# Kernel tuning notes

Hardware: AMD Instinct MI355X
Metric: run time of the kernel (lower is better)

## Reference

```python
import jax, jax.numpy as jnp
import numpy as np

N_NODES = 100_000
N_EDGES = 3_200_000
IN_DIM, HID_DIM, EMB_DIM = 128, 64, 32


def setup_inputs() -> dict:
    key = jax.random.key(0)
    k0, k1, k2, k3, k4, k5 = jax.random.split(key, 6)
    x = jax.random.normal(k0, (N_NODES, IN_DIM), dtype=jnp.float32)
    edge_index = jax.random.randint(k1, (2, N_EDGES), 0, N_NODES, dtype=jnp.int32)
    # GCNConv parameters (glorot-ish scale)
    W1 = jax.random.normal(k2, (IN_DIM, HID_DIM), dtype=jnp.float32) / np.sqrt(IN_DIM)
    b1 = jnp.zeros((HID_DIM,), dtype=jnp.float32)
    W2 = jax.random.normal(k3, (HID_DIM, EMB_DIM), dtype=jnp.float32) / np.sqrt(HID_DIM)
    b2 = jnp.zeros((EMB_DIM,), dtype=jnp.float32)
    return {"x": x, "W1": W1, "b1": b1, "W2": W2, "b2": b2, "edge_index": edge_index}


def reference(x, W1, b1, W2, b2, edge_index):
    """Two-layer GCN encoder (PyG GCNConv semantics, eval mode so dropout is a no-op).

    Each GCNConv: add self-loops, symmetric deg^-1/2 normalization,
    out = scatter_add(norm_e * (x @ W)[src], dst) + b.
    """
    N = x.shape[0]
    loops = jnp.arange(N, dtype=edge_index.dtype)
    src = jnp.concatenate([edge_index[0], loops])  # [E+N]
    dst = jnp.concatenate([edge_index[1], loops])  # [E+N]

    # degree of destination nodes (self-loops guarantee deg >= 1)
    deg = jax.ops.segment_sum(jnp.ones_like(dst, dtype=jnp.float32), dst,
                              num_segments=N)
    dinv = jax.lax.rsqrt(deg)                      # deg^-1/2, finite since deg>=1
    norm = dinv[src] * dinv[dst]                   # [E+N]

    def gcn_conv(h, W, b):
        h = h @ W                                  # dense transform [N, D_out]
        msg = h[src] * norm[:, None]               # gather + scale [E+N, D_out]
        return jax.ops.segment_sum(msg, dst, num_segments=N) + b

    h = jax.nn.relu(gcn_conv(x, W1, b1))
    # F.dropout with training=False is identity -> omitted
    return gcn_conv(h, W2, b2)
```

## Files before the change

kernel.cpp:

```cpp
#include <hip/hip_runtime.h>

static constexpr int NN = 100000;
static constexpr int NE = 3200000;
static constexpr int DI = 128;
static constexpr int DH = 64;
static constexpr int DO = 32;

static constexpr int NBK  = 391;
static constexpr int BCAP = 9216;
static constexpr int TILE = 8192;
static constexpr int NEB  = (NE + TILE - 1) / TILE;
static constexpr int NEBP = 392;
static constexpr int XW1_BASE = NEB + 1;
static constexpr int XW1_BLOCKS = (NN + 63) / 64;

typedef short short8 __attribute__((ext_vector_type(8)));
typedef float f32x4  __attribute__((ext_vector_type(4)));

__device__ __forceinline__ unsigned short f2bf(float f) {
    union { float f; unsigned u; } v; v.f = f;
    unsigned r = v.u + 0x7FFFu + ((v.u >> 16) & 1u);
    return (unsigned short)(r >> 16);
}
__device__ __forceinline__ float bflo(unsigned u) {
    union { unsigned u; float f; } v; v.u = u << 16; return v.f;
}
__device__ __forceinline__ float bfhi(unsigned u) {
    union { unsigned u; float f; } v; v.u = u & 0xFFFF0000u; return v.f;
}

__global__ __launch_bounds__(256) void k_count(
        const int* __restrict__ dst, int* __restrict__ cnt) {
    __shared__ int hist[NBK];
    int tid = threadIdx.x;
    for (int i = tid; i < NBK; i += 256) hist[i] = 0;
    __syncthreads();

    int base = blockIdx.x * TILE;
    int rem = NE - base;
#pragma unroll
    for (int k4 = 0; k4 < 8; ++k4) {
        int off = tid * 32 + k4 * 4;
        if (off < rem) {
            int4 d4 = *(const int4*)(dst + base + off);
            atomicAdd(&hist[(unsigned)d4.x >> 8], 1);
            atomicAdd(&hist[(unsigned)d4.y >> 8], 1);
            atomicAdd(&hist[(unsigned)d4.z >> 8], 1);
            atomicAdd(&hist[(unsigned)d4.w >> 8], 1);
        }
    }
    __syncthreads();
    for (int i = tid; i < NBK; i += 256)
        cnt[i * NEBP + blockIdx.x] = hist[i];
}

__global__ __launch_bounds__(64) void k_scan(
        int* __restrict__ cnt, int* __restrict__ bcur) {
    int b = blockIdx.x, tid = threadIdx.x;
    int* row = cnt + b * NEBP;
    int carry = 0;
    for (int c = 0; c < (NEB + 63) / 64; ++c) {
        int idx = c * 64 + tid;
        int v = (idx < NEB) ? row[idx] : 0;
        int inc = v;
#pragma unroll
        for (int o = 1; o < 64; o <<= 1) {
            int u = __shfl_up(inc, o, 64);
            if (tid >= o) inc += u;
        }
        int tot = __shfl(inc, 63, 64);
        if (idx < NEB) row[idx] = carry + inc - v;
        carry += tot;
    }
    if (tid == 0) bcur[b] = carry;
}

__global__ __launch_bounds__(256) void k_mega(
        const int* __restrict__ src, const int* __restrict__ dst,
        const int* __restrict__ gposM, int* __restrict__ bstore,
        const float* __restrict__ x, const float* __restrict__ W1,
        const float* __restrict__ W2,
        unsigned short* __restrict__ w2bf, unsigned short* __restrict__ h1b) {
    __shared__ int lcur[NBK];

    int tid = threadIdx.x;

    if (blockIdx.x < NEB) {
        for (int i = tid; i < NBK; i += 256)
            lcur[i] = gposM[i * NEBP + blockIdx.x];
        __syncthreads();

        int base = blockIdx.x * TILE;
        int rem = NE - base;
#pragma unroll
        for (int k4 = 0; k4 < 8; ++k4) {
            int off = tid * 32 + k4 * 4;
            if (off < rem) {
                int4 s4 = *(const int4*)(src + base + off);
                int4 d4 = *(const int4*)(dst + base + off);
                int b0 = (unsigned)d4.x >> 8, p0 = ((d4.x & 255) << 24) | s4.x;
                int b1 = (unsigned)d4.y >> 8, p1 = ((d4.y & 255) << 24) | s4.y;
                int b2 = (unsigned)d4.z >> 8, p2 = ((d4.z & 255) << 24) | s4.z;
                int b3 = (unsigned)d4.w >> 8, p3 = ((d4.w & 255) << 24) | s4.w;
                int o0 = atomicAdd(&lcur[b0], 1);
                int o1 = atomicAdd(&lcur[b1], 1);
                int o2 = atomicAdd(&lcur[b2], 1);
                int o3 = atomicAdd(&lcur[b3], 1);
                if (o0 < BCAP) bstore[b0 * BCAP + o0] = p0;
                if (o1 < BCAP) bstore[b1 * BCAP + o1] = p1;
                if (o2 < BCAP) bstore[b2 * BCAP + o2] = p2;
                if (o3 < BCAP) bstore[b3 * BCAP + o3] = p3;
            }
        }
    } else if (blockIdx.x == NEB) {
        for (int i = tid; i < DH * DO; i += 256) w2bf[i] = f2bf(W2[i]);
    } else {
        int wave = tid >> 6, lane = tid & 63;
        int q = lane >> 4, m = lane & 15, o0 = wave * 16;
        int nb = (blockIdx.x - XW1_BASE) * 64;

        short8 bfr[4];
#pragma unroll
        for (int kb = 0; kb < 4; ++kb)
#pragma unroll
            for (int j = 0; j < 8; ++j)
                bfr[kb][j] = (short)f2bf(W1[(kb * 32 + q * 8 + j) * DH + o0 + m]);

#pragma unroll
        for (int mt = 0; mt < 4; ++mt) {
            int row = min(nb + mt * 16 + m, NN - 1);
            const float* xr = x + (size_t)row * DI;
            f32x4 acc = {0.f, 0.f, 0.f, 0.f};
#pragma unroll
            for (int kb = 0; kb < 4; ++kb) {
                f32x4 u0 = *(const f32x4*)(xr + kb * 32 + q * 8);
                f32x4 u1 = *(const f32x4*)(xr + kb * 32 + q * 8 + 4);
                short8 a;
                a[0] = (short)f2bf(u0.x); a[1] = (short)f2bf(u0.y);
                a[2] = (short)f2bf(u0.z); a[3] = (short)f2bf(u0.w);
                a[4] = (short)f2bf(u1.x); a[5] = (short)f2bf(u1.y);
                a[6] = (short)f2bf(u1.z); a[7] = (short)f2bf(u1.w);
                acc = __builtin_amdgcn_mfma_f32_16x16x32_bf16(a, bfr[kb], acc, 0, 0, 0);
            }
#pragma unroll
            for (int r = 0; r < 4; ++r) {
                int n = nb + mt * 16 + q * 4 + r;
                if (n < NN) h1b[(size_t)n * DH + o0 + m] = f2bf(acc[r]);
            }
        }
    }
}

__global__ __launch_bounds__(512) void k_bsort(
        const int* __restrict__ bcur, int* __restrict__ bstore,
        int* __restrict__ rpb, int* __restrict__ rpe, float* __restrict__ dinv,
        unsigned* __restrict__ h1) {
    __shared__ int buf[BCAP];
    __shared__ int sorted[BCAP];
    __shared__ int hist[256], scan[256], cur[256];
    __shared__ float sdinv[256];

    int b = blockIdx.x, tid = threadIdx.x;
    int cnt = min(bcur[b], BCAP);
    int base = b * BCAP;
    for (int i = tid; i < cnt; i += 512) buf[i] = bstore[base + i];
    if (tid < 256) hist[tid] = 0;
    __syncthreads();
    for (int i = tid; i < cnt; i += 512)
        atomicAdd(&hist[((unsigned)buf[i]) >> 24], 1);
    __syncthreads();

    if (tid < 64) {
        int carry = 0;
        for (int c = 0; c < 4; ++c) {
            int idx = c * 64 + tid;
            int v = hist[idx];
            int inc = v;
#pragma unroll
            for (int o = 1; o < 64; o <<= 1) {
                int u = __shfl_up(inc, o, 64);
                if (tid >= o) inc += u;
            }
            int tot = __shfl(inc, 63, 64);
            scan[idx] = carry + inc - v;
            cur[idx]  = carry + inc - v;
            carry += tot;
        }
    }
    __syncthreads();

    if (tid < 256) {
        int n = b * 256 + tid;
        if (n < NN) {
            int beg = base + scan[tid];
            rpb[n] = beg;
            rpe[n] = beg + hist[tid];
            float dv = rsqrtf(1.0f + (float)hist[tid]);
            dinv[n] = dv;
            sdinv[tid] = dv;
        }
    }

    for (int i = tid; i < cnt; i += 512) {
        unsigned pv = (unsigned)buf[i];
        int pos = atomicAdd(&cur[pv >> 24], 1);
        sorted[pos] = (int)(pv & 0xFFFFFF);
    }
    __syncthreads();
    for (int i = tid; i < cnt; i += 512) bstore[base + i] = sorted[i];

    for (int i = tid; i < 2048; i += 512) {
        int r = i >> 3, n = b * 256 + r;
        if (n < NN) {
            float dv = sdinv[r];
            uint4* p = (uint4*)h1 + (size_t)b * 2048 + i;
            uint4 u = *p;
            u.x = (unsigned)f2bf(bflo(u.x) * dv) | ((unsigned)f2bf(bfhi(u.x) * dv) << 16);
            u.y = (unsigned)f2bf(bflo(u.y) * dv) | ((unsigned)f2bf(bfhi(u.y) * dv) << 16);
            u.z = (unsigned)f2bf(bflo(u.z) * dv) | ((unsigned)f2bf(bfhi(u.z) * dv) << 16);
            u.w = (unsigned)f2bf(bflo(u.w) * dv) | ((unsigned)f2bf(bfhi(u.w) * dv) << 16);
            *p = u;
        }
    }
}

__global__ __launch_bounds__(256) void k_gather64(
        const int* __restrict__ rpb, const int* __restrict__ rpe,
        const int* __restrict__ csr, const unsigned* __restrict__ h,
        const float* __restrict__ dinv, const float* __restrict__ b1,
        unsigned* __restrict__ tbf) {
    int wave = threadIdx.x >> 6, lane = threadIdx.x & 63;
    int q = lane >> 3, f8 = lane & 7;
    int n = blockIdx.x * 4 + wave;
    int beg = rpb[n], end = rpe[n];
    float dn = dinv[n];

    float s0 = 0.f, s1 = 0.f, s2 = 0.f, s3 = 0.f;
    float s4 = 0.f, s5 = 0.f, s6 = 0.f, s7 = 0.f;
    if (q == 0) {
        uint4 u = *(const uint4*)(h + (size_t)n * 32 + 4 * f8);
        s0 = bflo(u.x); s1 = bfhi(u.x); s2 = bflo(u.y); s3 = bfhi(u.y);
        s4 = bflo(u.z); s5 = bfhi(u.z); s6 = bflo(u.w); s7 = bfhi(u.w);
    }
#define ACC8(U)                                                         \
    s0 += bflo(U.x); s1 += bfhi(U.x); s2 += bflo(U.y); s3 += bfhi(U.y); \
    s4 += bflo(U.z); s5 += bfhi(U.z); s6 += bflo(U.w); s7 += bfhi(U.w);

    for (int c = beg; c < end; c += 64) {
        int cnt = min(64, end - c);
        int sidx = (lane < cnt) ? csr[c + lane] : 0;
        int j = 0;
        for (; j + 16 <= cnt; j += 16) {
            int sa = __shfl(sidx, j + q, 64);
            int sb = __shfl(sidx, j + 8 + q, 64);
            uint4 ua = *(const uint4*)(h + (size_t)sa * 32 + 4 * f8);
            uint4 ub = *(const uint4*)(h + (size_t)sb * 32 + 4 * f8);
            ACC8(ua) ACC8(ub)
        }
        for (; j + 8 <= cnt; j += 8) {
            int sa = __shfl(sidx, j + q, 64);
            uint4 ua = *(const uint4*)(h + (size_t)sa * 32 + 4 * f8);
            ACC8(ua)
        }
        for (; j < cnt; j += 8) {
            int slot = j + q;
            int s = __shfl(sidx, slot, 64);
            if (slot < cnt) {
                uint4 u = *(const uint4*)(h + (size_t)s * 32 + 4 * f8);
                ACC8(u)
            }
        }
    }
#undef ACC8

#define RED8(m)                                                         \
    s0 += __shfl_xor(s0, m, 64); s1 += __shfl_xor(s1, m, 64);           \
    s2 += __shfl_xor(s2, m, 64); s3 += __shfl_xor(s3, m, 64);           \
    s4 += __shfl_xor(s4, m, 64); s5 += __shfl_xor(s5, m, 64);           \
    s6 += __shfl_xor(s6, m, 64); s7 += __shfl_xor(s7, m, 64);
    RED8(8) RED8(16) RED8(32)
#undef RED8

    if (q == 0) {
        float4 bA = *(const float4*)(b1 + 8 * f8);
        float4 bB = *(const float4*)(b1 + 8 * f8 + 4);
        float t0 = fmaxf(fmaf(s0, dn, bA.x), 0.f);
        float t1 = fmaxf(fmaf(s1, dn, bA.y), 0.f);
        float t2 = fmaxf(fmaf(s2, dn, bA.z), 0.f);
        float t3 = fmaxf(fmaf(s3, dn, bA.w), 0.f);
        float t4 = fmaxf(fmaf(s4, dn, bB.x), 0.f);
        float t5 = fmaxf(fmaf(s5, dn, bB.y), 0.f);
        float t6 = fmaxf(fmaf(s6, dn, bB.z), 0.f);
        float t7 = fmaxf(fmaf(s7, dn, bB.w), 0.f);
        uint4 o;
        o.x = (unsigned)f2bf(t0) | ((unsigned)f2bf(t1) << 16);
        o.y = (unsigned)f2bf(t2) | ((unsigned)f2bf(t3) << 16);
        o.z = (unsigned)f2bf(t4) | ((unsigned)f2bf(t5) << 16);
        o.w = (unsigned)f2bf(t6) | ((unsigned)f2bf(t7) << 16);
        *(uint4*)(tbf + (size_t)n * 32 + 4 * f8) = o;
    }
}

__global__ __launch_bounds__(256) void k_l2_mfma(
        const unsigned short* __restrict__ tbf, const unsigned short* __restrict__ w2bf,
        const float* __restrict__ dinv, unsigned short* __restrict__ h2b) {
    int wave = threadIdx.x >> 6, lane = threadIdx.x & 63;
    int q = lane >> 4, m = lane & 15;
    int o0 = (wave & 1) * 16, mt = wave >> 1;
    int nb = blockIdx.x * 32;

    short8 bf[2];
#pragma unroll
    for (int kb = 0; kb < 2; ++kb)
#pragma unroll
        for (int j = 0; j < 8; ++j)
            bf[kb][j] = (short)w2bf[(kb * 32 + q * 8 + j) * DO + o0 + m];

    int row = nb + mt * 16 + m;
    f32x4 acc = {0.f, 0.f, 0.f, 0.f};
#pragma unroll
    for (int kb = 0; kb < 2; ++kb) {
        short8 a = *(const short8*)(tbf + (size_t)row * DH + kb * 32 + q * 8);
        acc = __builtin_amdgcn_mfma_f32_16x16x32_bf16(a, bf[kb], acc, 0, 0, 0);
    }
#pragma unroll
    for (int r = 0; r < 4; ++r) {
        int n = nb + mt * 16 + q * 4 + r;
        if (n < NN) h2b[(size_t)n * DO + o0 + m] = f2bf(acc[r] * dinv[n]);
    }
}

__global__ __launch_bounds__(256) void k_gather32(
        const int* __restrict__ rpb, const int* __restrict__ rpe,
        const int* __restrict__ csr, const unsigned* __restrict__ h,
        const float* __restrict__ dinv, const float* __restrict__ b2,
        float* __restrict__ out) {
    int wave = threadIdx.x >> 6, lane = threadIdx.x & 63;
    int q = lane >> 2, f4 = lane & 3;
    int n = blockIdx.x * 4 + wave;
    int beg = rpb[n], end = rpe[n];

    float s0 = 0.f, s1 = 0.f, s2 = 0.f, s3 = 0.f;
    float s4 = 0.f, s5 = 0.f, s6 = 0.f, s7 = 0.f;
    if (q == 0) {
        uint4 u = *(const uint4*)(h + (size_t)n * 16 + 4 * f4);
        s0 = bflo(u.x); s1 = bfhi(u.x); s2 = bflo(u.y); s3 = bfhi(u.y);
        s4 = bflo(u.z); s5 = bfhi(u.z); s6 = bflo(u.w); s7 = bfhi(u.w);
    }
#define ACC8(U)                                                         \
    s0 += bflo(U.x); s1 += bfhi(U.x); s2 += bflo(U.y); s3 += bfhi(U.y); \
    s4 += bflo(U.z); s5 += bfhi(U.z); s6 += bflo(U.w); s7 += bfhi(U.w);

    for (int c = beg; c < end; c += 64) {
        int cnt = min(64, end - c);
        int sidx = (lane < cnt) ? csr[c + lane] : 0;
        int j = 0;
        for (; j + 32 <= cnt; j += 32) {
            int sa = __shfl(sidx, j + q, 64);
            int sb = __shfl(sidx, j + 16 + q, 64);
            uint4 ua = *(const uint4*)(h + (size_t)sa * 16 + 4 * f4);
            uint4 ub = *(const uint4*)(h + (size_t)sb * 16 + 4 * f4);
            ACC8(ua) ACC8(ub)
        }
        for (; j + 16 <= cnt; j += 16) {
            int sa = __shfl(sidx, j + q, 64);
            uint4 ua = *(const uint4*)(h + (size_t)sa * 16 + 4 * f4);
            ACC8(ua)
        }
        for (; j < cnt; j += 16) {
            int slot = j + q;
            int s = __shfl(sidx, slot, 64);
            if (slot < cnt) {
                uint4 u = *(const uint4*)(h + (size_t)s * 16 + 4 * f4);
                ACC8(u)
            }
        }
    }
#undef ACC8

#define RED8(m)                                                         \
    s0 += __shfl_xor(s0, m, 64); s1 += __shfl_xor(s1, m, 64);           \
    s2 += __shfl_xor(s2, m, 64); s3 += __shfl_xor(s3, m, 64);           \
    s4 += __shfl_xor(s4, m, 64); s5 += __shfl_xor(s5, m, 64);           \
    s6 += __shfl_xor(s6, m, 64); s7 += __shfl_xor(s7, m, 64);
    RED8(4) RED8(8) RED8(16) RED8(32)
#undef RED8

    if (q == 0) {
        float dn = dinv[n];
        float4 bA = *(const float4*)(b2 + 8 * f4);
        float4 bB = *(const float4*)(b2 + 8 * f4 + 4);
        size_t o = (size_t)n * 32 + 8 * f4;
        float4 oA, oB;
        oA.x = fmaf(s0, dn, bA.x); oA.y = fmaf(s1, dn, bA.y);
        oA.z = fmaf(s2, dn, bA.z); oA.w = fmaf(s3, dn, bA.w);
        oB.x = fmaf(s4, dn, bB.x); oB.y = fmaf(s5, dn, bB.y);
        oB.z = fmaf(s6, dn, bB.z); oB.w = fmaf(s7, dn, bB.w);
        *(float4*)(out + o) = oA;
        *(float4*)(out + o + 4) = oB;
    }
}

extern "C" void kernel_launch(void* const* d_in, const int* in_sizes, int n_in,
                              void* d_out, int out_size, void* d_ws, size_t ws_size,
                              hipStream_t stream) {
    const float* x  = (const float*)d_in[0];
    const float* W1 = (const float*)d_in[1];
    const float* b1 = (const float*)d_in[2];
    const float* W2 = (const float*)d_in[3];
    const float* b2 = (const float*)d_in[4];
    const int* ei  = (const int*)d_in[5];
    const int* src = ei;
    const int* dst = ei + NE;
    float* out = (float*)d_out;

    float* ws    = (float*)d_ws;
    int*   rpb   = (int*)ws;
    int*   rpe   = (int*)(ws + 100352);
    float* dinv  = ws + 200704;
    int*   bcur  = (int*)(ws + 301056);
    int*   bstor = (int*)(ws + 301568);
    unsigned short* w2bf = (unsigned short*)(ws + 3905024);
    unsigned short* tbf  = (unsigned short*)(ws + 3906048);
    unsigned short* h1b  = (unsigned short*)(ws + 7106048);
    unsigned short* h2b  = h1b;
    int*   cntM  = (int*)tbf;

    k_count    <<<NEB, 256, 0, stream>>>(dst, cntM);
    k_scan     <<<NBK, 64, 0, stream>>>(cntM, bcur);
    k_mega     <<<XW1_BASE + XW1_BLOCKS, 256, 0, stream>>>(
                    src, dst, cntM, bstor, x, W1, W2, w2bf, h1b);
    k_bsort    <<<NBK, 512, 0, stream>>>(bcur, bstor, rpb, rpe, dinv,
                                         (unsigned*)h1b);

    k_gather64 <<<NN / 4, 256, 0, stream>>>(rpb, rpe, bstor, (const unsigned*)h1b,
                                            dinv, b1, (unsigned*)tbf);
    k_l2_mfma  <<<NN / 32, 256, 0, stream>>>(tbf, w2bf, dinv, h2b);
    k_gather32 <<<NN / 4, 256, 0, stream>>>(rpb, rpe, bstor, (const unsigned*)h2b,
                                            dinv, b2, out);
}
```

Measured before the change: 309.6 us.

## Replace count+scan passes with per-tile global atomic bucket reservation and LDS staging

```diff
diff --git a/kernel.cpp b/kernel.cpp
--- a/kernel.cpp
+++ b/kernel.cpp
@@ -9,10 +9,9 @@
 static constexpr int NBK  = 391;
 static constexpr int BCAP = 9216;
 static constexpr int TILE = 8192;
-static constexpr int NEB  = (NE + TILE - 1) / TILE;
-static constexpr int NEBP = 392;
-static constexpr int XW1_BASE = NEB + 1;
+static constexpr int XW1_BASE = 392;
 static constexpr int XW1_BLOCKS = (NN + 63) / 64;
+static constexpr int BSTRIDE = 16;
 
 typedef short short8 __attribute__((ext_vector_type(8)));
 typedef float f32x4  __attribute__((ext_vector_type(4)));
@@ -29,90 +28,82 @@
     union { unsigned u; float f; } v; v.u = u & 0xFFFF0000u; return v.f;
 }
 
-__global__ __launch_bounds__(256) void k_count(
-        const int* __restrict__ dst, int* __restrict__ cnt) {
-    __shared__ int hist[NBK];
-    int tid = threadIdx.x;
-    for (int i = tid; i < NBK; i += 256) hist[i] = 0;
-    __syncthreads();
-
-    int base = blockIdx.x * TILE;
-    int rem = NE - base;
-#pragma unroll
-    for (int k4 = 0; k4 < 8; ++k4) {
-        int off = tid * 32 + k4 * 4;
-        if (off < rem) {
-            int4 d4 = *(const int4*)(dst + base + off);
-            atomicAdd(&hist[(unsigned)d4.x >> 8], 1);
-            atomicAdd(&hist[(unsigned)d4.y >> 8], 1);
-            atomicAdd(&hist[(unsigned)d4.z >> 8], 1);
-            atomicAdd(&hist[(unsigned)d4.w >> 8], 1);
-        }
-    }
-    __syncthreads();
-    for (int i = tid; i < NBK; i += 256)
-        cnt[i * NEBP + blockIdx.x] = hist[i];
-}
-
-__global__ __launch_bounds__(64) void k_scan(
-        int* __restrict__ cnt, int* __restrict__ bcur) {
-    int b = blockIdx.x, tid = threadIdx.x;
-    int* row = cnt + b * NEBP;
-    int carry = 0;
-    for (int c = 0; c < (NEB + 63) / 64; ++c) {
-        int idx = c * 64 + tid;
-        int v = (idx < NEB) ? row[idx] : 0;
-        int inc = v;
-#pragma unroll
-        for (int o = 1; o < 64; o <<= 1) {
-            int u = __shfl_up(inc, o, 64);
-            if (tid >= o) inc += u;
-        }
-        int tot = __shfl(inc, 63, 64);
-        if (idx < NEB) row[idx] = carry + inc - v;
-        carry += tot;
-    }
-    if (tid == 0) bcur[b] = carry;
+__global__ void k_zero(int* __restrict__ p, int n) {
+    int i = blockIdx.x * blockDim.x + threadIdx.x;
+    if (i < n) p[i] = 0;
 }
 
 __global__ __launch_bounds__(256) void k_mega(
         const int* __restrict__ src, const int* __restrict__ dst,
-        const int* __restrict__ gposM, int* __restrict__ bstore,
+        int* __restrict__ bcurP, int* __restrict__ bstore,
         const float* __restrict__ x, const float* __restrict__ W1,
         const float* __restrict__ W2,
         unsigned short* __restrict__ w2bf, unsigned short* __restrict__ h1b) {
+    __shared__ int hist[NBK];
     __shared__ int lcur[NBK];
+    __shared__ int gpos[NBK];
+    __shared__ int stage[TILE];
+    __shared__ unsigned short bid[TILE];
 
     int tid = threadIdx.x;
 
-    if (blockIdx.x < NEB) {
+    if (blockIdx.x < NBK) {
+        for (int i = tid; i < NBK; i += 256) hist[i] = 0;
+        __syncthreads();
+
+        int base = blockIdx.x * TILE;
+        int p[32]; unsigned short bb[32];
+#pragma unroll
+        for (int k = 0; k < 32; ++k) {
+            int e = base + k * 256 + tid;
+            if (e < NE) {
+                int d = dst[e], s = src[e];
+                bb[k] = (unsigned short)(d >> 8);
+                p[k]  = ((d & 255) << 24) | s;
+                atomicAdd(&hist[bb[k]], 1);
+            } else bb[k] = 0xFFFF;
+        }
+        __syncthreads();
+
         for (int i = tid; i < NBK; i += 256)
-            lcur[i] = gposM[i * NEBP + blockIdx.x];
+            gpos[i] = atomicAdd(&bcurP[i * BSTRIDE], hist[i]);
         __syncthreads();
 
-        int base = blockIdx.x * TILE;
-        int rem = NE - base;
-#pragma unroll
-        for (int k4 = 0; k4 < 8; ++k4) {
-            int off = tid * 32 + k4 * 4;
-            if (off < rem) {
-                int4 s4 = *(const int4*)(src + base + off);
-                int4 d4 = *(const int4*)(dst + base + off);
-                int b0 = (unsigned)d4.x >> 8, p0 = ((d4.x & 255) << 24) | s4.x;
-                int b1 = (unsigned)d4.y >> 8, p1 = ((d4.y & 255) << 24) | s4.y;
-                int b2 = (unsigned)d4.z >> 8, p2 = ((d4.z & 255) << 24) | s4.z;
-                int b3 = (unsigned)d4.w >> 8, p3 = ((d4.w & 255) << 24) | s4.w;
-                int o0 = atomicAdd(&lcur[b0], 1);
-                int o1 = atomicAdd(&lcur[b1], 1);
-                int o2 = atomicAdd(&lcur[b2], 1);
-                int o3 = atomicAdd(&lcur[b3], 1);
-                if (o0 < BCAP) bstore[b0 * BCAP + o0] = p0;
-                if (o1 < BCAP) bstore[b1 * BCAP + o1] = p1;
-                if (o2 < BCAP) bstore[b2 * BCAP + o2] = p2;
-                if (o3 < BCAP) bstore[b3 * BCAP + o3] = p3;
-            }
-        }
-    } else if (blockIdx.x == NEB) {
+        if (tid < 64) {
+            int carry = 0;
+            for (int c = 0; c < (NBK + 63) / 64; ++c) {
+                int idx = c * 64 + tid;
+                int v = (idx < NBK) ? hist[idx] : 0;
+                int inc = v;
+#pragma unroll
+                for (int o = 1; o < 64; o <<= 1) {
+                    int u = __shfl_up(inc, o, 64);
+                    if (tid >= o) inc += u;
+                }
+                int tot = __shfl(inc, 63, 64);
+                if (idx < NBK) { int ex = carry + inc - v; hist[idx] = ex; lcur[idx] = ex; }
+                carry += tot;
+            }
+        }
+        __syncthreads();
+
+#pragma unroll
+        for (int k = 0; k < 32; ++k) {
+            if (bb[k] != 0xFFFF) {
+                int lp = atomicAdd(&lcur[bb[k]], 1);
+                stage[lp] = p[k];
+                bid[lp] = bb[k];
+            }
+        }
+        __syncthreads();
+
+        int tcnt = min(TILE, NE - base);
+        for (int i = tid; i < tcnt; i += 256) {
+            int b = bid[i];
+            int off = gpos[b] + (i - hist[b]);
+            if (off < BCAP) bstore[b * BCAP + off] = stage[i];
+        }
+    } else if (blockIdx.x == NBK) {
         for (int i = tid; i < DH * DO; i += 256) w2bf[i] = f2bf(W2[i]);
     } else {
         int wave = tid >> 6, lane = tid & 63;
@@ -152,7 +143,7 @@
 }
 
 __global__ __launch_bounds__(512) void k_bsort(
-        const int* __restrict__ bcur, int* __restrict__ bstore,
+        const int* __restrict__ bcurP, int* __restrict__ bstore,
         int* __restrict__ rpb, int* __restrict__ rpe, float* __restrict__ dinv,
         unsigned* __restrict__ h1) {
     __shared__ int buf[BCAP];
@@ -161,7 +152,7 @@
     __shared__ float sdinv[256];
 
     int b = blockIdx.x, tid = threadIdx.x;
-    int cnt = min(bcur[b], BCAP);
+    int cnt = min(bcurP[b * BSTRIDE], BCAP);
     int base = b * BCAP;
     for (int i = tid; i < cnt; i += 512) buf[i] = bstore[base + i];
     if (tid < 256) hist[tid] = 0;
@@ -418,19 +409,17 @@
     int*   rpb   = (int*)ws;
     int*   rpe   = (int*)(ws + 100352);
     float* dinv  = ws + 200704;
-    int*   bcur  = (int*)(ws + 301056);
     int*   bstor = (int*)(ws + 301568);
     unsigned short* w2bf = (unsigned short*)(ws + 3905024);
     unsigned short* tbf  = (unsigned short*)(ws + 3906048);
     unsigned short* h1b  = (unsigned short*)(ws + 7106048);
     unsigned short* h2b  = h1b;
-    int*   cntM  = (int*)tbf;
-
-    k_count    <<<NEB, 256, 0, stream>>>(dst, cntM);
-    k_scan     <<<NBK, 64, 0, stream>>>(cntM, bcur);
+    int*   bcurP = (int*)tbf;
+
+    k_zero     <<<25, 256, 0, stream>>>(bcurP, NBK * BSTRIDE);
     k_mega     <<<XW1_BASE + XW1_BLOCKS, 256, 0, stream>>>(
-                    src, dst, cntM, bstor, x, W1, W2, w2bf, h1b);
-    k_bsort    <<<NBK, 512, 0, stream>>>(bcur, bstor, rpb, rpe, dinv,
+                    src, dst, bcurP, bstor, x, W1, W2, w2bf, h1b);
+    k_bsort    <<<NBK, 512, 0, stream>>>(bcurP, bstor, rpb, rpe, dinv,
                                          (unsigned*)h1b);
 
     k_gather64 <<<NN / 4, 256, 0, stream>>>(rpb, rpe, bstor, (const unsigned*)h1b,
```

After: 273.7 us. 1.13x faster.
